# Performance work log

Measured on AMD Instinct MI355X. Metric: run time of the kernel, lower is better.

The kernel has to match this reference:

```python
import jax, jax.numpy as jnp
import numpy as np

EMBED_DIM = 2048
NUM_HEADS = 16
HEAD_DIM = EMBED_DIM // NUM_HEADS
SEQ_LEN = 2048
ROPE_BASE = 10000.0


def rope_cache(seq_len, dim, base=ROPE_BASE):
    inv_freq = 1.0 / (base ** (jnp.arange(0, dim, 2, dtype=jnp.float32) / dim))
    t = jnp.arange(seq_len, dtype=jnp.float32)
    freqs = jnp.einsum('s,d->sd', t, inv_freq)  # [S, D/2]
    return jnp.cos(freqs), jnp.sin(freqs)


def apply_rope_interleaved(x, cos, sin):
    # x: [B, S, H, D]; interleaved pairs (even, odd)
    B, S, H, D = x.shape
    xp = x.reshape(B, S, H, D // 2, 2)
    x1, x2 = xp[..., 0], xp[..., 1]
    c = cos[None, :, None, :]
    s = sin[None, :, None, :]
    o1 = x1 * c - x2 * s
    o2 = x1 * s + x2 * c
    return jnp.stack([o1, o2], axis=-1).reshape(B, S, H, D)


def setup_inputs() -> dict:
    key = jax.random.key(0)
    ks = jax.random.split(key, 5)
    B = 2
    scale = 0.02
    x = jax.random.normal(ks[0], (B, SEQ_LEN, EMBED_DIM), dtype=jnp.float32)
    Wq = jax.random.normal(ks[1], (EMBED_DIM, EMBED_DIM), dtype=jnp.float32) * scale
    Wk = jax.random.normal(ks[2], (EMBED_DIM, EMBED_DIM), dtype=jnp.float32) * scale
    Wv = jax.random.normal(ks[3], (EMBED_DIM, EMBED_DIM), dtype=jnp.float32) * scale
    Wo = jax.random.normal(ks[4], (EMBED_DIM, EMBED_DIM), dtype=jnp.float32) * scale
    return {"x": x, "Wq": Wq, "Wk": Wk, "Wv": Wv, "Wo": Wo}


def reference(x, Wq, Wk, Wv, Wo):
    B, S, E = x.shape
    H, D = NUM_HEADS, HEAD_DIM
    # projections (nn.Linear: y = x @ W.T; here W stored as [out, in])
    q = (x @ Wq.T).reshape(B, S, H, D)
    k = (x @ Wk.T).reshape(B, S, H, D)
    v = (x @ Wv.T).reshape(B, S, H, D)
    cos, sin = rope_cache(S, D)
    q = apply_rope_interleaved(q, cos, sin)
    k = apply_rope_interleaved(k, cos, sin)
    # causal attention, flash-attn semantics: scale = head_dim**-0.5, fp32 softmax
    scale = 1.0 / jnp.sqrt(jnp.float32(D))
    scores = jnp.einsum('bqhd,bkhd->bhqk', q, k) * scale
    causal = jnp.tril(jnp.ones((S, S), dtype=bool))
    scores = jnp.where(causal[None, None], scores, jnp.float32(-jnp.inf))
    probs = jax.nn.softmax(scores.astype(jnp.float32), axis=-1)
    attn = jnp.einsum('bhqk,bkhd->bqhd', probs.astype(v.dtype), v)
    attn = attn.reshape(B, S, H * D)
    return attn @ Wo.T
```

## Files before the change

### kernel.cpp

```cpp
#include <hip/hip_runtime.h>
#include <cstdint>
#include <cmath>

typedef short s16x8 __attribute__((ext_vector_type(8)));
typedef float f32x4 __attribute__((ext_vector_type(4)));
typedef float f32x16 __attribute__((ext_vector_type(16)));
typedef int   i32x4 __attribute__((ext_vector_type(4)));
typedef unsigned short u16;

#define E_DIM 2048
#define SEQ   2048
#define NB    2
#define NH    16
#define HD    128
#define BS_TOT 4096

__device__ __forceinline__ u16 f2bf(float f) {
  unsigned u = __float_as_uint(f);
  u += 0x7fffu + ((u >> 16) & 1u);
  return (u16)(u >> 16);
}
__device__ __forceinline__ float bf2f(u16 h) {
  return __uint_as_float(((unsigned)h) << 16);
}
__device__ __forceinline__ float rmax16(float v) {
  v = fmaxf(v, __shfl_xor(v, 1));
  v = fmaxf(v, __shfl_xor(v, 2));
  v = fmaxf(v, __shfl_xor(v, 4));
  v = fmaxf(v, __shfl_xor(v, 8));
  return v;
}
__device__ __forceinline__ float rsum16(float v) {
  v += __shfl_xor(v, 1);
  v += __shfl_xor(v, 2);
  v += __shfl_xor(v, 4);
  v += __shfl_xor(v, 8);
  return v;
}

__device__ __forceinline__ void gll16(const u16* g, u16* l) {
  __builtin_amdgcn_global_load_lds(
      (const __attribute__((address_space(1))) void*)g,
      (__attribute__((address_space(3))) void*)l, 16, 0, 0);
}

__global__ __launch_bounds__(256) void cast_kernel(const float* __restrict__ in,
                                                   u16* __restrict__ out) {
  const size_t t = (size_t)blockIdx.x * 256 + threadIdx.x;
  const float* p = in + t * 8;
  f32x4 a = *(const f32x4*)p;
  f32x4 b = *(const f32x4*)(p + 4);
  union { u16 u[8]; i32x4 v; } r;
  r.u[0] = f2bf(a[0]); r.u[1] = f2bf(a[1]); r.u[2] = f2bf(a[2]); r.u[3] = f2bf(a[3]);
  r.u[4] = f2bf(b[0]); r.u[5] = f2bf(b[1]); r.u[6] = f2bf(b[2]); r.u[7] = f2bf(b[3]);
  *(i32x4*)(out + t * 8) = r.v;
}

__global__ __launch_bounds__(256) void cast2_kernel(const float* __restrict__ in0,
                                                    u16* __restrict__ out0,
                                                    const float* __restrict__ in1,
                                                    u16* __restrict__ out1,
                                                    int half) {
  const int bsel = blockIdx.x >= half;
  const float* in = bsel ? in1 : in0;
  u16* out = bsel ? out1 : out0;
  const size_t t = (size_t)(blockIdx.x - (bsel ? half : 0)) * 256 + threadIdx.x;
  const float* p = in + t * 8;
  f32x4 a = *(const f32x4*)p;
  f32x4 b = *(const f32x4*)(p + 4);
  union { u16 u[8]; i32x4 v; } r;
  r.u[0] = f2bf(a[0]); r.u[1] = f2bf(a[1]); r.u[2] = f2bf(a[2]); r.u[3] = f2bf(a[3]);
  r.u[4] = f2bf(b[0]); r.u[5] = f2bf(b[1]); r.u[6] = f2bf(b[2]); r.u[7] = f2bf(b[3]);
  *(i32x4*)(out + t * 8) = r.v;
}

template <typename OT, bool CVTA>
__global__ __launch_bounds__(256) void gemm_nt(const void* __restrict__ Av,
                                               const u16* __restrict__ B,
                                               OT* __restrict__ C,
                                               int M, int N, int K) {
  __shared__ __align__(16) u16 As[128 * 64];
  __shared__ __align__(16) u16 Bs[128 * 64];
  const int t  = threadIdx.x;
  const int w  = t >> 6, l = t & 63;
  const int l31 = l & 31, lh = l >> 5;
  const int wr = w >> 1, wc = w & 1;
  const int m0 = blockIdx.y * 128, n0 = blockIdx.x * 128;

  f32x16 acc[2][2];
#pragma unroll
  for (int mi = 0; mi < 2; ++mi)
#pragma unroll
    for (int ni = 0; ni < 2; ++ni)
#pragma unroll
      for (int e = 0; e < 16; ++e) acc[mi][ni][e] = 0.f;

  for (int k0 = 0; k0 < K; k0 += 64) {
    __syncthreads();
    if constexpr (CVTA) {
      const float* A = (const float*)Av;
#pragma unroll
      for (int i = 0; i < 4; ++i) {
        const int ci = i * 256 + t;
        const int r = ci >> 3, c = ci & 7, gq = c ^ (r & 7);
        const float* s = A + (size_t)(m0 + r) * K + k0 + gq * 8;
        f32x4 a = *(const f32x4*)s;
        f32x4 b = *(const f32x4*)(s + 4);
        union { u16 u[8]; i32x4 v; } rr;
        rr.u[0] = f2bf(a[0]); rr.u[1] = f2bf(a[1]); rr.u[2] = f2bf(a[2]); rr.u[3] = f2bf(a[3]);
        rr.u[4] = f2bf(b[0]); rr.u[5] = f2bf(b[1]); rr.u[6] = f2bf(b[2]); rr.u[7] = f2bf(b[3]);
        *(i32x4*)(As + ci * 8) = rr.v;
      }
    } else {
      const u16* A = (const u16*)Av;
#pragma unroll
      for (int i = 0; i < 4; ++i) {
        const int ci = i * 256 + t;
        const int r = ci >> 3, c = ci & 7, gq = c ^ (r & 7);
        gll16(A + (size_t)(m0 + r) * K + k0 + gq * 8, As + ci * 8);
      }
    }
#pragma unroll
    for (int i = 0; i < 4; ++i) {
      const int ci = i * 256 + t;
      const int r = ci >> 3, c = ci & 7, gq = c ^ (r & 7);
      gll16(B + (size_t)(n0 + r) * K + k0 + gq * 8, Bs + ci * 8);
    }
    __syncthreads();
#pragma unroll
    for (int ks = 0; ks < 4; ++ks) {
      const int chunk = ks * 2 + lh;
      s16x8 af[2], bf[2];
#pragma unroll
      for (int mi = 0; mi < 2; ++mi) {
        const int ra = wr * 64 + mi * 32 + l31;
        af[mi] = *(const s16x8*)(As + ra * 64 + ((chunk ^ (ra & 7)) << 3));
      }
#pragma unroll
      for (int ni = 0; ni < 2; ++ni) {
        const int rb = wc * 64 + ni * 32 + l31;
        bf[ni] = *(const s16x8*)(Bs + rb * 64 + ((chunk ^ (rb & 7)) << 3));
      }
#pragma unroll
      for (int mi = 0; mi < 2; ++mi)
#pragma unroll
        for (int ni = 0; ni < 2; ++ni)
          acc[mi][ni] = __builtin_amdgcn_mfma_f32_32x32x16_bf16(af[mi], bf[ni], acc[mi][ni], 0, 0, 0);
    }
  }

#pragma unroll
  for (int mi = 0; mi < 2; ++mi)
#pragma unroll
    for (int ni = 0; ni < 2; ++ni) {
      const int col = n0 + wc * 64 + ni * 32 + l31;
#pragma unroll
      for (int reg = 0; reg < 16; ++reg) {
        const int row = m0 + wr * 64 + mi * 32 + 4 * lh + (reg & 3) + 8 * (reg >> 2);
        const float v = acc[mi][ni][reg];
        if constexpr (sizeof(OT) == 2) {
          C[(size_t)row * N + col] = (OT)f2bf(v);
        } else {
          C[(size_t)row * N + col] = v;
        }
      }
    }
}

__global__ __launch_bounds__(256) void gemm_qk(const u16* __restrict__ A,
                                               const u16* __restrict__ B0,
                                               const u16* __restrict__ B1,
                                               u16* __restrict__ C0,
                                               u16* __restrict__ C1) {
  constexpr int K = 2048, N = 2048;
  __shared__ __align__(16) u16 As[128 * 64];
  __shared__ __align__(16) u16 Bs[128 * 64];
  const int bx = blockIdx.x;
  const u16* B = (bx >> 4) ? B1 : B0;
  u16* C = (bx >> 4) ? C1 : C0;
  const int n0 = (bx & 15) * 128, m0 = blockIdx.y * 128;
  const int t  = threadIdx.x;
  const int w  = t >> 6, l = t & 63;
  const int l31 = l & 31, lh = l >> 5;
  const int wr = w >> 1, wc = w & 1;

  f32x16 acc[2][2];
#pragma unroll
  for (int mi = 0; mi < 2; ++mi)
#pragma unroll
    for (int ni = 0; ni < 2; ++ni)
#pragma unroll
      for (int e = 0; e < 16; ++e) acc[mi][ni][e] = 0.f;

  for (int k0 = 0; k0 < K; k0 += 64) {
    __syncthreads();
#pragma unroll
    for (int i = 0; i < 4; ++i) {
      const int ci = i * 256 + t;
      const int r = ci >> 3, c = ci & 7, gq = c ^ (r & 7);
      gll16(A + (size_t)(m0 + r) * K + k0 + gq * 8, As + ci * 8);
    }
#pragma unroll
    for (int i = 0; i < 4; ++i) {
      const int ci = i * 256 + t;
      const int r = ci >> 3, c = ci & 7, gq = c ^ (r & 7);
      gll16(B + (size_t)(n0 + r) * K + k0 + gq * 8, Bs + ci * 8);
    }
    __syncthreads();
#pragma unroll
    for (int ks = 0; ks < 4; ++ks) {
      const int chunk = ks * 2 + lh;
      s16x8 af[2], bf[2];
#pragma unroll
      for (int mi = 0; mi < 2; ++mi) {
        const int ra = wr * 64 + mi * 32 + l31;
        af[mi] = *(const s16x8*)(As + ra * 64 + ((chunk ^ (ra & 7)) << 3));
      }
#pragma unroll
      for (int ni = 0; ni < 2; ++ni) {
        const int rb = wc * 64 + ni * 32 + l31;
        bf[ni] = *(const s16x8*)(Bs + rb * 64 + ((chunk ^ (rb & 7)) << 3));
      }
#pragma unroll
      for (int mi = 0; mi < 2; ++mi)
#pragma unroll
        for (int ni = 0; ni < 2; ++ni)
          acc[mi][ni] = __builtin_amdgcn_mfma_f32_32x32x16_bf16(af[mi], bf[ni], acc[mi][ni], 0, 0, 0);
    }
  }

#pragma unroll
  for (int mi = 0; mi < 2; ++mi)
#pragma unroll
    for (int ni = 0; ni < 2; ++ni) {
      const int col = n0 + wc * 64 + ni * 32 + l31;
#pragma unroll
      for (int reg = 0; reg < 16; ++reg) {
        const int row = m0 + wr * 64 + mi * 32 + 4 * lh + (reg & 3) + 8 * (reg >> 2);
        C[(size_t)row * N + col] = f2bf(acc[mi][ni][reg]);
      }
    }
}

__global__ __launch_bounds__(256) void rope_kernel(u16* __restrict__ q, u16* __restrict__ k) {
  const float QS = 0.08838834764831845f * 1.4426950408889634f;
  const size_t t = (size_t)blockIdx.x * 256 + threadIdx.x;
  const size_t e8 = t * 8;
  const int col = (int)(e8 & (E_DIM - 1));
  const int row = (int)(e8 >> 11);
  const int s   = row & (SEQ - 1);
  const int d   = col & (HD - 1);
  float cs[4], sn[4];
#pragma unroll
  for (int j = 0; j < 4; ++j) {
    const float inv = exp2f(-0.20762050593046014f * (float)((d >> 1) + j));
    const float ang = (float)s * inv;
    sincosf(ang, &sn[j], &cs[j]);
  }
  u16* qp = q + e8;
  u16* kp = k + e8;
  union { u16 u[8]; i32x4 v; } a, b;
  a.v = *(const i32x4*)qp;
  b.v = *(const i32x4*)kp;
#pragma unroll
  for (int j = 0; j < 4; ++j) {
    const float csq = cs[j] * QS, snq = sn[j] * QS;
    const float q1 = bf2f(a.u[2 * j]), q2 = bf2f(a.u[2 * j + 1]);
    const float k1 = bf2f(b.u[2 * j]), k2 = bf2f(b.u[2 * j + 1]);
    a.u[2 * j]     = f2bf(q1 * csq - q2 * snq);
    a.u[2 * j + 1] = f2bf(q1 * snq + q2 * csq);
    b.u[2 * j]     = f2bf(k1 * cs[j] - k2 * sn[j]);
    b.u[2 * j + 1] = f2bf(k1 * sn[j] + k2 * cs[j]);
  }
  *(i32x4*)qp = a.v;
  *(i32x4*)kp = b.v;
}

__global__ __launch_bounds__(256, 2) void flash_kernel(const u16* __restrict__ q,
                                                       const u16* __restrict__ kmat,
                                                       const u16* __restrict__ vt,
                                                       u16* __restrict__ attn) {
  __shared__ __align__(16) u16 KV[32768];
  const int bx = blockIdx.x;
  const int j = bx & 15, h = (bx >> 4) & 15, b = bx >> 8;
  const int t = threadIdx.x, w = t >> 6, l = t & 63, lq = l >> 4, lm = l & 15;

  u16* myP = KV + w * 2048;
  const u16* kbase = kmat + (size_t)(b * SEQ) * E_DIM + h * HD;
  const u16* vbase = vt + (size_t)(h * HD) * BS_TOT + (size_t)b * SEQ;
  const f32x4 fzero = {0.f, 0.f, 0.f, 0.f};

  for (int pass = 0; pass < 2; ++pass) {
    const int qt = pass ? j : (31 - j);
    const int q0 = qt * 64;
    const int nT = (qt >> 1) + 1;

    const u16* qp = q + (size_t)(b * SEQ + q0 + w * 16) * E_DIM + h * HD;
    s16x8 qf[4];
#pragma unroll
    for (int kx = 0; kx < 4; ++kx)
      qf[kx] = *(const s16x8*)(qp + (size_t)lm * E_DIM + kx * 32 + lq * 8);

    float m_i[4], l_i[4];
    f32x4 acc_o[8];
#pragma unroll
    for (int rr = 0; rr < 4; ++rr) { m_i[rr] = -1e30f; l_i[rr] = 0.f; }
#pragma unroll
    for (int nd = 0; nd < 8; ++nd) acc_o[nd] = fzero;

    for (int it = 0; it < nT; ++it) {
      const int k0 = it * 128;
      __syncthreads();
#pragma unroll
      for (int i = 0; i < 8; ++i) {
        const int ci = i * 256 + t;
        const int r = ci >> 4, gq = (ci & 15) ^ (r & 15);
        gll16(kbase + (size_t)(k0 + r) * E_DIM + gq * 8, KV + ci * 8);
      }
#pragma unroll
      for (int i = 0; i < 8; ++i) {
        const int ci = i * 256 + t;
        const int r = ci >> 4, gq = (ci & 15) ^ (r & 15);
        gll16(vbase + (size_t)r * BS_TOT + k0 + gq * 8, KV + 16384 + ci * 8);
      }
      __syncthreads();

      f32x4 sc[8];
#pragma unroll
      for (int ni = 0; ni < 8; ++ni) sc[ni] = fzero;
#pragma unroll
      for (int kx = 0; kx < 4; ++kx) {
        s16x8 kf[8];
#pragma unroll
        for (int ni = 0; ni < 8; ++ni) {
          const int rn = ni * 16 + lm;
          kf[ni] = *(const s16x8*)(KV + rn * 128 + (((kx * 4 + lq) ^ lm) << 3));
        }
#pragma unroll
        for (int ni = 0; ni < 8; ++ni)
          sc[ni] = __builtin_amdgcn_mfma_f32_16x16x32_bf16(qf[kx], kf[ni], sc[ni], 0, 0, 0);
      }

      const bool diag = (it == nT - 1);
#pragma unroll
      for (int rr = 0; rr < 4; ++rr) {
        const int qrow = q0 + w * 16 + lq * 4 + rr;
        float mt = -1e30f;
#pragma unroll
        for (int ni = 0; ni < 8; ++ni) {
          float s = sc[ni][rr];
          if (diag && (k0 + ni * 16 + lm) > qrow) s = -1e30f;
          sc[ni][rr] = s;
          mt = fmaxf(mt, s);
        }
        mt = rmax16(mt);
        const float mn = fmaxf(m_i[rr], mt);
        const float al = exp2f(m_i[rr] - mn);
        float rs = 0.f;
#pragma unroll
        for (int ni = 0; ni < 8; ++ni) {
          const float p = exp2f(sc[ni][rr] - mn);
          sc[ni][rr] = p;
          rs += p;
        }
        rs = rsum16(rs);
        l_i[rr] = l_i[rr] * al + rs;
        m_i[rr] = mn;
#pragma unroll
        for (int nd = 0; nd < 8; ++nd) acc_o[nd][rr] *= al;
      }

      __syncthreads();
#pragma unroll
      for (int rr = 0; rr < 4; ++rr) {
        const int r = lq * 4 + rr;
#pragma unroll
        for (int ni = 0; ni < 8; ++ni) {
          const int c = ni * 16 + lm;
          myP[r * 128 + (((c >> 3) ^ r) << 3) + (c & 7)] = f2bf(sc[ni][rr]);
        }
      }

#pragma unroll
      for (int kx = 0; kx < 4; ++kx) {
        const s16x8 pf = *(const s16x8*)(myP + lm * 128 + (((kx * 4 + lq) ^ lm) << 3));
#pragma unroll
        for (int nd = 0; nd < 8; ++nd) {
          const int rn = nd * 16 + lm;
          const s16x8 vf = *(const s16x8*)(KV + 16384 + rn * 128 + (((kx * 4 + lq) ^ lm) << 3));
          acc_o[nd] = __builtin_amdgcn_mfma_f32_16x16x32_bf16(pf, vf, acc_o[nd], 0, 0, 0);
        }
      }
    }

    u16* op = attn + (size_t)(b * SEQ + q0 + w * 16) * E_DIM + h * HD;
#pragma unroll
    for (int rr = 0; rr < 4; ++rr) {
      const float inv = 1.0f / l_i[rr];
      const int row = lq * 4 + rr;
#pragma unroll
      for (int nd = 0; nd < 8; ++nd) {
        const int colc = nd * 16 + lm;
        op[(size_t)row * E_DIM + colc] = f2bf(acc_o[nd][rr] * inv);
      }
    }
  }
}

extern "C" void kernel_launch(void* const* d_in, const int* in_sizes, int n_in,
                              void* d_out, int out_size, void* d_ws, size_t ws_size,
                              hipStream_t stream) {
  const float* x  = (const float*)d_in[0];
  const float* Wq = (const float*)d_in[1];
  const float* Wk = (const float*)d_in[2];
  const float* Wv = (const float*)d_in[3];
  const float* Wo = (const float*)d_in[4];
  float* out = (float*)d_out;
  char* ws = (char*)d_ws;

  u16* xb    = (u16*)(ws);
  u16* vslot = (u16*)(ws + (size_t)16 * 1048576);
  u16* wq_bf = vslot;
  u16* wk_bf = vslot + (size_t)4 * 1048576;
  u16* vtb   = vslot;
  u16* wo_bf = vslot;
  u16* qb    = (u16*)d_out;
  u16* kb    = (u16*)d_out + (size_t)8 * 1048576;
  u16* attnb = xb;

  (void)in_sizes; (void)n_in; (void)out_size; (void)ws_size;

  cast_kernel<<<4096, 256, 0, stream>>>(x, xb);
  cast2_kernel<<<4096, 256, 0, stream>>>(Wq, wq_bf, Wk, wk_bf, 2048);
  gemm_qk<<<dim3(32, 32), 256, 0, stream>>>(xb, wq_bf, wk_bf, qb, kb);
  gemm_nt<u16, true><<<dim3(32, 16), 256, 0, stream>>>(Wv, xb, vtb, 2048, 4096, 2048);
  rope_kernel<<<4096, 256, 0, stream>>>(qb, kb);
  flash_kernel<<<512, 256, 0, stream>>>(qb, kb, vtb, attnb);
  cast_kernel<<<2048, 256, 0, stream>>>(Wo, wo_bf);
  gemm_nt<float, false><<<dim3(16, 32), 256, 0, stream>>>(attnb, wo_bf, out, 4096, 2048, 2048);
}
```

Baseline: 438.4 us.

## Double-buffer K/V tiles in flash attention with 512-thread blocks and 128-row queries

Restructures the flash attention kernel to use 8 waves per block, each covering a 128-row query tile. K/V tiles are double-buffered in 64K elements of LDS, and the next tile is prefetched with async global-to-LDS loads while the current one is computed. Waits use vmcnt plus raw s_barrier, MFMA sections get raised wave priority, and block indices are remapped so heads are interleaved across the grid. This aims to hide global load latency and cut barrier stalls, but doubles LDS use (128KB) per block, which may limit occupancy and makes the manual vmcnt counting fragile.

```diff
diff --git a/kernel.cpp b/kernel.cpp
--- a/kernel.cpp
+++ b/kernel.cpp
@@ -276,24 +276,44 @@
   *(i32x4*)kp = b.v;
 }
 
-__global__ __launch_bounds__(256, 2) void flash_kernel(const u16* __restrict__ q,
+__global__ __launch_bounds__(512, 2) void flash_kernel(const u16* __restrict__ q,
                                                        const u16* __restrict__ kmat,
                                                        const u16* __restrict__ vt,
                                                        u16* __restrict__ attn) {
-  __shared__ __align__(16) u16 KV[32768];
+  __shared__ __align__(16) u16 KV[65536];
   const int bx = blockIdx.x;
-  const int j = bx & 15, h = (bx >> 4) & 15, b = bx >> 8;
+  const int j  = bx >> 5;
+  const int bh = (bx & 7) * 4 + ((bx >> 3) & 3);
+  const int b  = bh >> 4, h = bh & 15;
   const int t = threadIdx.x, w = t >> 6, l = t & 63, lq = l >> 4, lm = l & 15;
 
-  u16* myP = KV + w * 2048;
   const u16* kbase = kmat + (size_t)(b * SEQ) * E_DIM + h * HD;
   const u16* vbase = vt + (size_t)(h * HD) * BS_TOT + (size_t)b * SEQ;
   const f32x4 fzero = {0.f, 0.f, 0.f, 0.f};
 
+  auto stage = [&](int it) {
+    const int base = (it & 1) << 15;
+    const int k0 = it * 128;
+#pragma unroll
+    for (int i = 0; i < 4; ++i) {
+      const int ci = i * 512 + t;
+      const int r = ci >> 4, gq = (ci & 15) ^ (r & 15);
+      gll16(kbase + (size_t)(k0 + r) * E_DIM + gq * 8, KV + base + ci * 8);
+    }
+#pragma unroll
+    for (int i = 0; i < 4; ++i) {
+      const int ci = i * 512 + t;
+      const int r = ci >> 4, gq = (ci & 15) ^ (r & 15);
+      gll16(vbase + (size_t)r * BS_TOT + k0 + gq * 8, KV + base + 16384 + ci * 8);
+    }
+  };
+
   for (int pass = 0; pass < 2; ++pass) {
-    const int qt = pass ? j : (31 - j);
-    const int q0 = qt * 64;
-    const int nT = (qt >> 1) + 1;
+    const int qt = pass ? j : (15 - j);
+    const int q0 = qt * 128;
+    const int nT = qt + 1;
+
+    stage(0);
 
     const u16* qp = q + (size_t)(b * SEQ + q0 + w * 16) * E_DIM + h * HD;
     s16x8 qf[4];
@@ -309,37 +329,33 @@
     for (int nd = 0; nd < 8; ++nd) acc_o[nd] = fzero;
 
     for (int it = 0; it < nT; ++it) {
+      const int base = (it & 1) << 15;
       const int k0 = it * 128;
-      __syncthreads();
-#pragma unroll
-      for (int i = 0; i < 8; ++i) {
-        const int ci = i * 256 + t;
-        const int r = ci >> 4, gq = (ci & 15) ^ (r & 15);
-        gll16(kbase + (size_t)(k0 + r) * E_DIM + gq * 8, KV + ci * 8);
-      }
-#pragma unroll
-      for (int i = 0; i < 8; ++i) {
-        const int ci = i * 256 + t;
-        const int r = ci >> 4, gq = (ci & 15) ^ (r & 15);
-        gll16(vbase + (size_t)r * BS_TOT + k0 + gq * 8, KV + 16384 + ci * 8);
-      }
-      __syncthreads();
+      if (it + 1 < nT) {
+        stage(it + 1);
+        asm volatile("s_waitcnt vmcnt(8)" ::: "memory");
+      } else {
+        asm volatile("s_waitcnt vmcnt(0)" ::: "memory");
+      }
+      asm volatile("s_barrier" ::: "memory");
 
       f32x4 sc[8];
 #pragma unroll
       for (int ni = 0; ni < 8; ++ni) sc[ni] = fzero;
+      __builtin_amdgcn_s_setprio(1);
 #pragma unroll
       for (int kx = 0; kx < 4; ++kx) {
         s16x8 kf[8];
 #pragma unroll
         for (int ni = 0; ni < 8; ++ni) {
           const int rn = ni * 16 + lm;
-          kf[ni] = *(const s16x8*)(KV + rn * 128 + (((kx * 4 + lq) ^ lm) << 3));
+          kf[ni] = *(const s16x8*)(KV + base + rn * 128 + (((kx * 4 + lq) ^ lm) << 3));
         }
 #pragma unroll
         for (int ni = 0; ni < 8; ++ni)
           sc[ni] = __builtin_amdgcn_mfma_f32_16x16x32_bf16(qf[kx], kf[ni], sc[ni], 0, 0, 0);
       }
+      __builtin_amdgcn_s_setprio(0);
 
       const bool diag = (it == nT - 1);
 #pragma unroll
@@ -370,27 +386,32 @@
         for (int nd = 0; nd < 8; ++nd) acc_o[nd][rr] *= al;
       }
 
-      __syncthreads();
+      asm volatile("s_barrier" ::: "memory");
+      u16* P = KV + base + w * 2048;
 #pragma unroll
       for (int rr = 0; rr < 4; ++rr) {
         const int r = lq * 4 + rr;
 #pragma unroll
         for (int ni = 0; ni < 8; ++ni) {
           const int c = ni * 16 + lm;
-          myP[r * 128 + (((c >> 3) ^ r) << 3) + (c & 7)] = f2bf(sc[ni][rr]);
-        }
-      }
-
+          P[r * 128 + (((c >> 3) ^ r) << 3) + (c & 7)] = f2bf(sc[ni][rr]);
+        }
+      }
+
+      __builtin_amdgcn_s_setprio(1);
 #pragma unroll
       for (int kx = 0; kx < 4; ++kx) {
-        const s16x8 pf = *(const s16x8*)(myP + lm * 128 + (((kx * 4 + lq) ^ lm) << 3));
+        const s16x8 pf = *(const s16x8*)(P + lm * 128 + (((kx * 4 + lq) ^ lm) << 3));
 #pragma unroll
         for (int nd = 0; nd < 8; ++nd) {
           const int rn = nd * 16 + lm;
-          const s16x8 vf = *(const s16x8*)(KV + 16384 + rn * 128 + (((kx * 4 + lq) ^ lm) << 3));
+          const s16x8 vf = *(const s16x8*)(KV + base + 16384 + rn * 128 + (((kx * 4 + lq) ^ lm) << 3));
           acc_o[nd] = __builtin_amdgcn_mfma_f32_16x16x32_bf16(pf, vf, acc_o[nd], 0, 0, 0);
         }
       }
+      __builtin_amdgcn_s_setprio(0);
+
+      asm volatile("s_barrier" ::: "memory");
     }
 
     u16* op = attn + (size_t)(b * SEQ + q0 + w * 16) * E_DIM + h * HD;
@@ -435,7 +456,7 @@
   gemm_qk<<<dim3(32, 32), 256, 0, stream>>>(xb, wq_bf, wk_bf, qb, kb);
   gemm_nt<u16, true><<<dim3(32, 16), 256, 0, stream>>>(Wv, xb, vtb, 2048, 4096, 2048);
   rope_kernel<<<4096, 256, 0, stream>>>(qb, kb);
-  flash_kernel<<<512, 256, 0, stream>>>(qb, kb, vtb, attnb);
+  flash_kernel<<<256, 512, 0, stream>>>(qb, kb, vtb, attnb);
   cast_kernel<<<2048, 256, 0, stream>>>(Wo, wo_bf);
   gemm_nt<float, false><<<dim3(16, 32), 256, 0, stream>>>(attnb, wo_bf, out, 4096, 2048, 2048);
 }
```

Result: faster. 419.6 us (-4.3%).
